# Optimization experiments

Hardware: AMD Instinct MI355X
Metric: run time of the kernel (lower is better)

Reference implementation:

```python
import jax, jax.numpy as jnp
import numpy as np
from jax import lax

H = 1024
NH = 16
R = 32
B, S = 32, 1024
LN_EPS = 1e-5

def _gelu(x):
    return jax.nn.gelu(x, approximate=False)

def setup_inputs() -> dict:
    key = jax.random.key(0)
    ks = jax.random.split(key, 24)
    w = lambda k, shape: jax.random.normal(k, shape, jnp.float32) * 0.02
    d = {}
    d['computation_results'] = jax.random.normal(ks[0], (B, S, H), jnp.float32)
    d['max_steps'] = 16
    # rule selector: Linear(H,H), GELU, Linear(H,R)
    d['rule_w1'] = w(ks[1], (H, H)); d['rule_b1'] = jnp.zeros((H,))
    d['rule_w2'] = w(ks[2], (R, H)); d['rule_b2'] = jnp.zeros((R,))
    d['rule_emb'] = jax.random.normal(ks[3], (R, H), jnp.float32)
    # MultiheadAttention packed in-proj [3H,H] and out-proj [H,H]
    d['attn_in_w'] = w(ks[4], (3 * H, H)); d['attn_in_b'] = jnp.zeros((3 * H,))
    d['attn_out_w'] = w(ks[5], (H, H)); d['attn_out_b'] = jnp.zeros((H,))
    # 2-layer LSTM, PyTorch gate order i,f,g,o
    d['lstm_wih0'] = w(ks[6], (4 * H, H)); d['lstm_whh0'] = w(ks[7], (4 * H, H))
    d['lstm_bih0'] = jnp.zeros((4 * H,)); d['lstm_bhh0'] = jnp.zeros((4 * H,))
    d['lstm_wih1'] = w(ks[8], (4 * H, H)); d['lstm_whh1'] = w(ks[9], (4 * H, H))
    d['lstm_bih1'] = jnp.zeros((4 * H,)); d['lstm_bhh1'] = jnp.zeros((4 * H,))
    # step generator: Linear(H,2H), LayerNorm(2H), GELU, Linear(2H,H)
    d['gen_w1'] = w(ks[10], (2 * H, H)); d['gen_b1'] = jnp.zeros((2 * H,))
    d['gen_ln_g'] = jnp.ones((2 * H,)); d['gen_ln_b'] = jnp.zeros((2 * H,))
    d['gen_w2'] = w(ks[11], (H, 2 * H)); d['gen_b2'] = jnp.zeros((H,))
    # step validator: Linear(2H,H), GELU, Linear(H,1), Sigmoid
    d['val_w1'] = w(ks[12], (H, 2 * H)); d['val_b1'] = jnp.zeros((H,))
    d['val_w2'] = w(ks[13], (1, H)); d['val_b2'] = jnp.zeros((1,))
    # proof verifier: Linear(H,H), GELU, Linear(H,1), Sigmoid
    d['ver_w1'] = w(ks[14], (H, H)); d['ver_b1'] = jnp.zeros((H,))
    d['ver_w2'] = w(ks[15], (1, H)); d['ver_b2'] = jnp.zeros((1,))
    return d


def reference(computation_results, max_steps, rule_w1, rule_b1, rule_w2, rule_b2, rule_emb,
              attn_in_w, attn_in_b, attn_out_w, attn_out_b,
              lstm_wih0, lstm_whh0, lstm_bih0, lstm_bhh0,
              lstm_wih1, lstm_whh1, lstm_bih1, lstm_bhh1,
              gen_w1, gen_b1, gen_ln_g, gen_ln_b, gen_w2, gen_b2,
              val_w1, val_b1, val_w2, val_b2,
              ver_w1, ver_b1, ver_w2, ver_b2):
    comp = computation_results
    b, s, h = comp.shape
    dh = h // NH
    scale = dh ** -0.5
    wq, wk, wv = jnp.split(attn_in_w, 3, axis=0)
    bq, bk, bv = jnp.split(attn_in_b, 3, axis=0)
    # K/V projections of the static context, computed once outside the step loop
    K = (comp @ wk.T + bk).reshape(b, s, NH, dh)  # [B,S,NH,dh]
    V = (comp @ wv.T + bv).reshape(b, s, NH, dh)
    lstm_params = ((lstm_wih0, lstm_whh0, lstm_bih0, lstm_bhh0),
                   (lstm_wih1, lstm_whh1, lstm_bih1, lstm_bhh1))

    def step(carry, _):
        ps, hmem, cmem = carry  # ps: [B,H]; hmem/cmem: [2,B,H]
        # rule selection
        logits = _gelu(ps @ rule_w1.T + rule_b1) @ rule_w2.T + rule_b2
        probs = jax.nn.softmax(logits, axis=-1)  # [B,R]
        sel = probs @ rule_emb  # [B,H]
        # single-query multi-head attention over computation context
        q = (ps @ wq.T + bq).reshape(b, NH, dh) * scale
        scores = jnp.einsum('bhd,bshd->bhs', q, K)
        a = jax.nn.softmax(scores, axis=-1)  # [B,NH,S]
        ctx = jnp.einsum('bhs,bshd->bhd', a, V).reshape(b, h) @ attn_out_w.T + attn_out_b
        attn_avg = a.mean(axis=1)  # head-averaged weights, [B,S]
        # 2-layer LSTM cell, one timestep
        x = ps
        hs, cs = [], []
        for l, (wih, whh, bih, bhh) in enumerate(lstm_params):
            g = x @ wih.T + bih + hmem[l] @ whh.T + bhh
            gi, gf, gg, go = jnp.split(g, 4, axis=-1)
            cn = jax.nn.sigmoid(gf) * cmem[l] + jax.nn.sigmoid(gi) * jnp.tanh(gg)
            hn = jax.nn.sigmoid(go) * jnp.tanh(cn)
            hs.append(hn); cs.append(cn); x = hn
        mem_out = x
        # step generator with LayerNorm+GELU
        si = ps + sel + ctx + mem_out
        z = si @ gen_w1.T + gen_b1
        mu = z.mean(axis=-1, keepdims=True)
        var = ((z - mu) ** 2).mean(axis=-1, keepdims=True)
        z = (z - mu) / jnp.sqrt(var + LN_EPS) * gen_ln_g + gen_ln_b
        nxt = _gelu(z) @ gen_w2.T + gen_b2
        val = jax.nn.sigmoid(_gelu(jnp.concatenate([ps, nxt], axis=-1) @ val_w1.T + val_b1) @ val_w2.T + val_b2)
        return (nxt, jnp.stack(hs), jnp.stack(cs)), (nxt, probs, val, attn_avg)

    init_state = comp[:, 0, :]
    carry0 = (init_state, jnp.zeros((2, b, h), comp.dtype), jnp.zeros((2, b, h), comp.dtype))
    (final, _, _), (steps, probs, vals, attn) = lax.scan(step, carry0, None, length=int(max_steps))
    proof_steps = jnp.concatenate([init_state[None], steps], axis=0)  # [T+1,B,H]
    proof_validity = jax.nn.sigmoid(_gelu(final @ ver_w1.T + ver_b1) @ ver_w2.T + ver_b2)  # [B,1]
    return proof_steps, proof_validity, probs, vals, attn
```

## Files before the change

kernel.cpp:

```cpp
#include <hip/hip_runtime.h>

typedef unsigned short u16;
typedef unsigned int u32;
typedef __attribute__((ext_vector_type(8))) short short8v;
typedef __attribute__((ext_vector_type(4))) float f32x4;

#define MFMA16(a,b,c) __builtin_amdgcn_mfma_f32_16x16x32_bf16((a),(b),(c),0,0,0)

__device__ __forceinline__ u16 f2bf(float f){
  u32 u = __float_as_uint(f);
  return (u16)((u + 0x7fffu + ((u >> 16) & 1u)) >> 16);
}
__device__ __forceinline__ float bf2f(u16 h){ return __uint_as_float(((u32)h) << 16); }
__device__ __forceinline__ float gelu_f(float x){ return 0.5f * x * (1.f + erff(x * 0.70710678118654752f)); }
__device__ __forceinline__ float sigm_f(float x){ return 1.f / (1.f + __expf(-x)); }
__device__ __forceinline__ void acc4(float4& a, const float4 b){ a.x+=b.x; a.y+=b.y; a.z+=b.z; a.w+=b.w; }

__device__ __forceinline__ void gl16(const void* g, void* l){
  __builtin_amdgcn_global_load_lds((const __attribute__((address_space(1))) u32*)g,
                                   (__attribute__((address_space(3))) u32*)l, 16, 0, 0);
}

struct CastJobs { const float* s[12]; u16* d[12]; int start[13]; };
__global__ __launch_bounds__(256) void cast_all_k(CastJobs J){
  int bx = blockIdx.x, j = 0;
  #pragma unroll
  for (int t = 0; t < 12; t++) if (bx >= J.start[t + 1]) j = t + 1;
  int i = (bx - J.start[j]) * 1024 + threadIdx.x * 4;
  float4 v = *(const float4*)(J.s[j] + i);
  ushort4 o; o.x = f2bf(v.x); o.y = f2bf(v.y); o.z = f2bf(v.z); o.w = f2bf(v.w);
  *(ushort4*)(J.d[j] + i) = o;
}

__global__ __launch_bounds__(256) void cast_k(const float* __restrict__ s, u16* __restrict__ d, int n){
  int i = (blockIdx.x * 256 + threadIdx.x) * 4;
  if (i + 3 < n){
    float4 v = *(const float4*)(s + i);
    ushort4 o; o.x = f2bf(v.x); o.y = f2bf(v.y); o.z = f2bf(v.z); o.w = f2bf(v.w);
    *(ushort4*)(d + i) = o;
  }
}

__global__ __launch_bounds__(256) void tcast_k(const float* __restrict__ s, u16* __restrict__ d){
  __shared__ float tile[32][33];
  int bx = blockIdx.x & 31, by = blockIdx.x >> 5;
  int tx = threadIdx.x & 31, ty = threadIdx.x >> 5;
  #pragma unroll
  for (int i = 0; i < 4; i++)
    tile[ty + i * 8][tx] = s[(size_t)(by * 32 + ty + i * 8) * 1024 + bx * 32 + tx];
  __syncthreads();
  #pragma unroll
  for (int i = 0; i < 4; i++)
    d[(size_t)(bx * 32 + ty + i * 8) * 1024 + by * 32 + tx] = f2bf(tile[tx][ty + i * 8]);
}

__global__ __launch_bounds__(256) void bias2_k(const float* __restrict__ gw1, const float* __restrict__ aob,
                                               const float* __restrict__ gb1, float* __restrict__ out){
  int j = blockIdx.x * 32 + (threadIdx.x >> 3);
  int l8 = threadIdx.x & 7;
  const float* r = gw1 + (size_t)j * 1024;
  float acc = 0.f;
  #pragma unroll 8
  for (int kk = 0; kk < 32; kk++){
    int k = kk * 32 + l8 * 4;
    float4 a = *(const float4*)(r + k);
    float4 w = *(const float4*)(aob + k);
    acc += a.x * w.x + a.y * w.y + a.z * w.z + a.w * w.w;
  }
  acc += __shfl_xor(acc, 1); acc += __shfl_xor(acc, 2); acc += __shfl_xor(acc, 4);
  if (l8 == 0) out[j] = gb1[j] + acc;
}

__global__ __launch_bounds__(256) void init_k(const float* __restrict__ comp, float* ps0, float* outp,
                                              float* h0, float* c0, float* h1, float* c1){
  int i = blockIdx.x * 256 + threadIdx.x;
  int b = i >> 10, hh = i & 1023;
  float v = comp[(size_t)b * 1048576 + hh];
  ps0[i] = v; outp[i] = v;
  h0[i] = 0.f; c0[i] = 0.f; h1[i] = 0.f; c1[i] = 0.f;
}

__global__ __launch_bounds__(256) void gemmkv_k(const u16* __restrict__ compb,
    const u16* __restrict__ Wk, const u16* __restrict__ Wv,
    const float* __restrict__ bk, const float* __restrict__ bv,
    u16* __restrict__ Kt, u16* __restrict__ Vb)
{
  __shared__ u16 Sh[16384];
  u16* As = Sh;
  u16* Bs = Sh + 8192;
  int tid = threadIdx.x;
  int x = blockIdx.x;
  int xcd = x & 7, p = x >> 3;
  int cpanel = xcd * 32 + (p >> 3);
  int wpanel = p & 7;
  int isK = (blockIdx.z != 0);
  const u16 *msrc, *nsrc; int m0, n0;
  if (!isK){ m0 = cpanel * 128; n0 = wpanel * 128; msrc = compb; nsrc = Wv; }
  else     { m0 = wpanel * 128; n0 = cpanel * 128; msrc = Wk;    nsrc = compb; }

  int w = tid >> 6, l = tid & 63, lr = l & 15, lk = l >> 4;
  int wm = (w >> 1) * 64, wn = (w & 1) * 64;
  f32x4 acc[4][4];
  #pragma unroll
  for (int i = 0; i < 4; i++)
    #pragma unroll
    for (int j = 0; j < 4; j++) acc[i][j] = (f32x4){0.f,0.f,0.f,0.f};

  for (int kc = 0; kc < 1024; kc += 64){
    #pragma unroll
    for (int r = 0; r < 4; r++){
      int s = tid + r * 256;
      int row = s >> 3, pp = s & 7;
      int lg = pp ^ (row & 7);
      gl16(msrc + (size_t)(m0 + row) * 1024 + kc + lg * 8, As + s * 8);
      gl16(nsrc + (size_t)(n0 + row) * 1024 + kc + lg * 8, Bs + s * 8);
    }
    __syncthreads();
    #pragma unroll
    for (int kk = 0; kk < 2; kk++){
      short8v a[4], bb[4];
      #pragma unroll
      for (int mi = 0; mi < 4; mi++){
        int row = wm + mi * 16 + lr;
        int ph = (kk * 4 + lk) ^ (row & 7);
        a[mi] = *(const short8v*)(As + row * 64 + ph * 8);
      }
      #pragma unroll
      for (int ni = 0; ni < 4; ni++){
        int row = wn + ni * 16 + lr;
        int ph = (kk * 4 + lk) ^ (row & 7);
        bb[ni] = *(const short8v*)(Bs + row * 64 + ph * 8);
      }
      #pragma unroll
      for (int mi = 0; mi < 4; mi++)
        #pragma unroll
        for (int ni = 0; ni < 4; ni++)
          acc[mi][ni] = MFMA16(a[mi], bb[ni], acc[mi][ni]);
    }
    __syncthreads();
  }
  #pragma unroll
  for (int mi = 0; mi < 4; mi++)
    #pragma unroll
    for (int ni = 0; ni < 4; ni++)
      #pragma unroll
      for (int r = 0; r < 4; r++){
        int row = wm + mi * 16 + lk * 4 + r;
        int col = wn + ni * 16 + lr;
        float bias = isK ? bk[m0 + row] : bv[n0 + col];
        Sh[row * 128 + col] = f2bf(acc[mi][ni][r] + bias);
      }
  __syncthreads();
  u16* dst = isK ? Kt : Vb;
  size_t base = isK ? (((size_t)(n0 >> 10) * 1024 + m0) * 1024 + (n0 & 1023))
                    : ((size_t)m0 * 1024 + n0);
  for (int i = tid; i < 2048; i += 256){
    int r = i >> 4, c8 = (i & 15) * 8;
    *(uint4*)(dst + base + (size_t)r * 1024 + c8) = *(const uint4*)(Sh + r * 128 + c8);
  }
}

__global__ __launch_bounds__(256) void gemmbb_k(const u16* __restrict__ A, const u16* __restrict__ B,
                                                u16* __restrict__ C)
{
  __shared__ u16 As[128 * 64];
  __shared__ u16 Bs[128 * 64];
  int tid = threadIdx.x;
  int m0 = blockIdx.x * 128, n0 = blockIdx.y * 128;
  int w = tid >> 6, l = tid & 63, lr = l & 15, lk = l >> 4;
  int wm = (w >> 1) * 64, wn = (w & 1) * 64;
  f32x4 acc[4][4];
  #pragma unroll
  for (int i = 0; i < 4; i++)
    #pragma unroll
    for (int j = 0; j < 4; j++) acc[i][j] = (f32x4){0.f,0.f,0.f,0.f};
  for (int kc = 0; kc < 1024; kc += 64){
    #pragma unroll
    for (int r = 0; r < 4; r++){
      int s = tid + r * 256;
      int row = s >> 3, pp = s & 7;
      int lg = pp ^ (row & 7);
      gl16(A + (size_t)(m0 + row) * 1024 + kc + lg * 8, As + s * 8);
      gl16(B + (size_t)(n0 + row) * 1024 + kc + lg * 8, Bs + s * 8);
    }
    __syncthreads();
    #pragma unroll
    for (int kk = 0; kk < 2; kk++){
      short8v a[4], bb[4];
      #pragma unroll
      for (int mi = 0; mi < 4; mi++){
        int row = wm + mi * 16 + lr;
        int ph = (kk * 4 + lk) ^ (row & 7);
        a[mi] = *(const short8v*)(As + row * 64 + ph * 8);
      }
      #pragma unroll
      for (int ni = 0; ni < 4; ni++){
        int row = wn + ni * 16 + lr;
        int ph = (kk * 4 + lk) ^ (row & 7);
        bb[ni] = *(const short8v*)(Bs + row * 64 + ph * 8);
      }
      #pragma unroll
      for (int mi = 0; mi < 4; mi++)
        #pragma unroll
        for (int ni = 0; ni < 4; ni++)
          acc[mi][ni] = MFMA16(a[mi], bb[ni], acc[mi][ni]);
    }
    __syncthreads();
  }
  #pragma unroll
  for (int mi = 0; mi < 4; mi++)
    #pragma unroll
    for (int ni = 0; ni < 4; ni++)
      #pragma unroll
      for (int r = 0; r < 4; r++){
        int row = m0 + wm + mi * 16 + lk * 4 + r;
        int col = n0 + wn + ni * 16 + lr;
        C[(size_t)row * 1024 + col] = f2bf(acc[mi][ni][r]);
      }
}

struct LinSeg {
  const float* X0; const float* Xa; const float* Xb; const float* Xc;
  const u16* W1; const float* b1;
  const float* Y; const u16* W2; const float* b2;
  float* out; float* out2;
  int K1, ld1, K2, ld2, N, act, gate;
  float scale;
  float* stats;
  const float* lng; const float* lnb; const float* lnstats;
  const float* cprev; float* cout; float* hout;
};

__device__ __forceinline__ short8v pack8(float4 v0, float4 v1){
  short8v r;
  r[0]=(short)f2bf(v0.x); r[1]=(short)f2bf(v0.y); r[2]=(short)f2bf(v0.z); r[3]=(short)f2bf(v0.w);
  r[4]=(short)f2bf(v1.x); r[5]=(short)f2bf(v1.y); r[6]=(short)f2bf(v1.z); r[7]=(short)f2bf(v1.w);
  return r;
}

__device__ __forceinline__ short8v load_sum8(const LinSeg& S, int row, int kb){
  size_t o = (size_t)row * S.K1 + kb;
  float4 v0 = *(const float4*)(S.X0 + o);
  float4 v1 = *(const float4*)(S.X0 + o + 4);
  if (S.lng){
    float mu = S.lnstats[row] * (1.f / 2048.f);
    float ms = S.lnstats[32 + row] * (1.f / 2048.f);
    float rstd = rsqrtf(ms - mu * mu + 1e-5f);
    float4 g0 = *(const float4*)(S.lng + kb), g1 = *(const float4*)(S.lng + kb + 4);
    float4 b0 = *(const float4*)(S.lnb + kb), b1 = *(const float4*)(S.lnb + kb + 4);
    v0.x = gelu_f((v0.x - mu) * rstd * g0.x + b0.x);
    v0.y = gelu_f((v0.y - mu) * rstd * g0.y + b0.y);
    v0.z = gelu_f((v0.z - mu) * rstd * g0.z + b0.z);
    v0.w = gelu_f((v0.w - mu) * rstd * g0.w + b0.w);
    v1.x = gelu_f((v1.x - mu) * rstd * g1.x + b1.x);
    v1.y = gelu_f((v1.y - mu) * rstd * g1.y + b1.y);
    v1.z = gelu_f((v1.z - mu) * rstd * g1.z + b1.z);
    v1.w = gelu_f((v1.w - mu) * rstd * g1.w + b1.w);
  } else {
    if (S.Xa){ acc4(v0, *(const float4*)(S.Xa + o)); acc4(v1, *(const float4*)(S.Xa + o + 4)); }
    if (S.Xb){ acc4(v0, *(const float4*)(S.Xb + o)); acc4(v1, *(const float4*)(S.Xb + o + 4)); }
    if (S.Xc){ acc4(v0, *(const float4*)(S.Xc + o)); acc4(v1, *(const float4*)(S.Xc + o + 4)); }
  }
  return pack8(v0, v1);
}
__device__ __forceinline__ short8v load_y8(const float* p){
  return pack8(*(const float4*)(p), *(const float4*)(p + 4));
}

typedef float Red4[32][32];

__device__ void lin_body(const LinSeg& S, int bi, int tid, Red4* red){
  int c0 = bi * 32, j0 = bi * 8;
  int w = tid >> 6, l = tid & 63, lr = l & 15, lk = l >> 4;
  int wc0 = S.gate ? ((lr >> 3) << 10) + j0 + (lr & 7) : c0 + lr;
  int wc1 = S.gate ? (((lr + 16) >> 3) << 10) + j0 + ((lr + 16) & 7) : c0 + lr + 16;
  f32x4 acc[2][2];
  #pragma unroll
  for (int i = 0; i < 2; i++)
    #pragma unroll
    for (int j = 0; j < 2; j++) acc[i][j] = (f32x4){0.f,0.f,0.f,0.f};

  {
    int chunk = S.K1 >> 2;
    int kb0 = w * chunk + lk * 8;
    for (int kk = 0; kk < chunk; kk += 32){
      int kb = kb0 + kk;
      short8v a0 = load_sum8(S, lr, kb);
      short8v a1 = load_sum8(S, lr + 16, kb);
      short8v w0 = *(const short8v*)(S.W1 + (size_t)wc0 * S.ld1 + kb);
      short8v w1 = *(const short8v*)(S.W1 + (size_t)wc1 * S.ld1 + kb);
      acc[0][0] = MFMA16(a0, w0, acc[0][0]);
      acc[0][1] = MFMA16(a0, w1, acc[0][1]);
      acc[1][0] = MFMA16(a1, w0, acc[1][0]);
      acc[1][1] = MFMA16(a1, w1, acc[1][1]);
    }
  }
  if (S.Y){
    int chunk = S.K2 >> 2;
    int kb0 = w * chunk + lk * 8;
    for (int kk = 0; kk < chunk; kk += 32){
      int kb = kb0 + kk;
      short8v a0 = load_y8(S.Y + (size_t)lr * S.K2 + kb);
      short8v a1 = load_y8(S.Y + (size_t)(lr + 16) * S.K2 + kb);
      short8v w0 = *(const short8v*)(S.W2 + (size_t)wc0 * S.ld2 + kb);
      short8v w1 = *(const short8v*)(S.W2 + (size_t)wc1 * S.ld2 + kb);
      acc[0][0] = MFMA16(a0, w0, acc[0][0]);
      acc[0][1] = MFMA16(a0, w1, acc[0][1]);
      acc[1][0] = MFMA16(a1, w0, acc[1][0]);
      acc[1][1] = MFMA16(a1, w1, acc[1][1]);
    }
  }
  #pragma unroll
  for (int mi = 0; mi < 2; mi++)
    #pragma unroll
    for (int ni = 0; ni < 2; ni++)
      #pragma unroll
      for (int r = 0; r < 4; r++)
        red[w][mi * 16 + lk * 4 + r][ni * 16 + lr] = acc[mi][ni][r];
  __syncthreads();
  if (S.gate){
    int row = tid >> 3, j = tid & 7;
    float s[4];
    #pragma unroll
    for (int g = 0; g < 4; g++){
      float v = 0.f;
      #pragma unroll
      for (int ww = 0; ww < 4; ww++) v += red[ww][row][g * 8 + j];
      s[g] = v;
    }
    int gc = j0 + j;
    float gI = s[0] + S.b1[gc]        + S.b2[gc];
    float gF = s[1] + S.b1[1024 + gc] + S.b2[1024 + gc];
    float gG = s[2] + S.b1[2048 + gc] + S.b2[2048 + gc];
    float gO = s[3] + S.b1[3072 + gc] + S.b2[3072 + gc];
    int idx = row * 1024 + gc;
    float cN = sigm_f(gF) * S.cprev[idx] + sigm_f(gI) * tanhf(gG);
    S.cout[idx] = cN;
    S.hout[idx] = sigm_f(gO) * tanhf(cN);
    return;
  }
  float vout[4]; int iout[4];
  int cnt = 0;
  for (int i = tid; i < 1024; i += 256){
    int row = i >> 5, col = i & 31;
    float v = 0.f;
    #pragma unroll
    for (int ww = 0; ww < 4; ww++) v += red[ww][row][col];
    v += S.b1[c0 + col];
    if (S.b2) v += S.b2[c0 + col];
    if (S.act == 1) v = gelu_f(v);
    else if (S.act == 2) v *= S.scale;
    S.out[(size_t)row * S.N + c0 + col] = v;
    if (S.out2) S.out2[(size_t)row * S.N + c0 + col] = v;
    vout[cnt] = v; iout[cnt] = i; cnt++;
  }
  if (S.stats){
    __syncthreads();
    float* rf = (float*)red;
    #pragma unroll
    for (int q2 = 0; q2 < 4; q2++){
      rf[iout[q2]] = vout[q2];
      rf[1024 + iout[q2]] = vout[q2] * vout[q2];
    }
    __syncthreads();
    if (tid < 32){
      float s = 0.f, s2 = 0.f;
      #pragma unroll
      for (int cc = 0; cc < 32; cc++){ s += rf[tid * 32 + cc]; s2 += rf[1024 + tid * 32 + cc]; }
      atomicAdd(S.stats + tid, s);
      atomicAdd(S.stats + 32 + tid, s2);
    }
  }
}

__global__ __launch_bounds__(256) void linmulti_k(LinSeg s0, LinSeg s1, LinSeg s2, int n0, int n1){
  __shared__ float red[4][32][32];
  int bx = blockIdx.x, tid = threadIdx.x;
  if (bx < n0) lin_body(s0, bx, tid, red);
  else if (bx < n0 + n1) lin_body(s1, bx - n0, tid, red);
  else lin_body(s2, bx - n0 - n1, tid, red);
}

__device__ void attn_job(int bh, int tid, const float* q, const u16* Kt, const u16* Vb,
                         float* afull, float* ctx0, float* shf){
  float* qs = shf;
  float* sc = shf + 64;
  float* rmx = shf + 1088;
  float* rsm = shf + 1092;
  float* ctxp = shf + 1096;
  int b = bh >> 4, h = bh & 15;
  if (tid < 64) qs[tid] = q[bh * 64 + tid];
  __syncthreads();
  const u32* kt = (const u32*)(Kt + (size_t)bh * 65536);
  float a0 = 0.f, a1 = 0.f, a2 = 0.f, a3 = 0.f;
  #pragma unroll 8
  for (int d = 0; d < 64; d++){
    float qd = qs[d];
    u32 p0 = kt[d * 512 + tid];
    u32 p1 = kt[d * 512 + tid + 256];
    a0 += qd * bf2f((u16)(p0 & 0xffff)); a1 += qd * bf2f((u16)(p0 >> 16));
    a2 += qd * bf2f((u16)(p1 & 0xffff)); a3 += qd * bf2f((u16)(p1 >> 16));
  }
  float mx = fmaxf(fmaxf(a0, a1), fmaxf(a2, a3));
  for (int o = 1; o < 64; o <<= 1) mx = fmaxf(mx, __shfl_xor(mx, o));
  if ((tid & 63) == 0) rmx[tid >> 6] = mx;
  __syncthreads();
  mx = fmaxf(fmaxf(rmx[0], rmx[1]), fmaxf(rmx[2], rmx[3]));
  float e0 = __expf(a0 - mx), e1 = __expf(a1 - mx), e2 = __expf(a2 - mx), e3 = __expf(a3 - mx);
  float sm = e0 + e1 + e2 + e3;
  for (int o = 1; o < 64; o <<= 1) sm += __shfl_xor(sm, o);
  if ((tid & 63) == 0) rsm[tid >> 6] = sm;
  __syncthreads();
  sm = rsm[0] + rsm[1] + rsm[2] + rsm[3];
  float inv = 1.f / sm;
  float* ar = afull + (size_t)bh * 1024;
  float2 w0 = make_float2(e0 * inv, e1 * inv);
  float2 w1 = make_float2(e2 * inv, e3 * inv);
  *(float2*)(sc + 2 * tid) = w0;       *(float2*)(ar + 2 * tid) = w0;
  *(float2*)(sc + 512 + 2 * tid) = w1; *(float2*)(ar + 512 + 2 * tid) = w1;
  __syncthreads();
  int d2 = (tid & 31) * 2, chunk = tid >> 5;
  const u16* vb = Vb + ((size_t)(b * 1024) * 16 + h) * 64 + d2;
  float c0 = 0.f, c1 = 0.f;
  for (int s = chunk * 128; s < chunk * 128 + 128; s++){
    u32 vv = *(const u32*)(vb + (size_t)s * 1024);
    float wv = sc[s];
    c0 += wv * bf2f((u16)(vv & 0xffff));
    c1 += wv * bf2f((u16)(vv >> 16));
  }
  *(float2*)(ctxp + chunk * 64 + d2) = make_float2(c0, c1);
  __syncthreads();
  if (tid < 64){
    float r = 0.f;
    #pragma unroll
    for (int c = 0; c < 8; c++) r += ctxp[c * 64 + tid];
    ctx0[bh * 64 + tid] = r;
  }
}

__device__ void rule2_job(int b, int tid, const float* h1a, const float* w2, const float* b2,
                          const float* emb, float* probs_out, float* sel, float* shf){
  float* lg = shf;
  float* psh = shf + 32;
  int j = tid >> 3, l8 = tid & 7;
  const float* xr = h1a + b * 1024;
  const float* wr = w2 + j * 1024;
  float acc = 0.f;
  #pragma unroll 8
  for (int kk = 0; kk < 32; kk++){
    int k = kk * 32 + l8 * 4;
    float4 xv = *(const float4*)(xr + k);
    float4 wv = *(const float4*)(wr + k);
    acc += xv.x * wv.x + xv.y * wv.y + xv.z * wv.z + xv.w * wv.w;
  }
  acc += __shfl_xor(acc, 1); acc += __shfl_xor(acc, 2); acc += __shfl_xor(acc, 4);
  if (l8 == 0) lg[j] = acc + b2[j];
  __syncthreads();
  if (tid < 32){
    float v = lg[tid];
    float m = v;
    for (int o = 1; o < 32; o <<= 1) m = fmaxf(m, __shfl_xor(m, o));
    float e = __expf(v - m);
    float s = e;
    for (int o = 1; o < 32; o <<= 1) s += __shfl_xor(s, o);
    float p = e / s;
    psh[tid] = p;
    probs_out[b * 32 + tid] = p;
  }
  __syncthreads();
  for (int j2 = tid; j2 < 1024; j2 += 256){
    float a2 = 0.f;
    #pragma unroll
    for (int r = 0; r < 32; r++) a2 += psh[r] * emb[r * 1024 + j2];
    sel[b * 1024 + j2] = a2;
  }
}

struct D2Params {
  const float* qbuf;
  const u16* Kt; const u16* Vb; float* afull; float* ctx0;
  const float* h1a; const float* w2; const float* b2r; const float* emb;
  float* probs_out; float* sel;
  LinSeg sL1; float* lnstats;
};
__global__ __launch_bounds__(256) void step_d2_k(D2Params P){
  __shared__ float red[4][32][32];
  float* shf = &red[0][0][0];
  int bx = blockIdx.x, tid = threadIdx.x;
  if (bx < 512){ attn_job(bx, tid, P.qbuf, P.Kt, P.Vb, P.afull, P.ctx0, shf); return; }
  if (bx < 544){ rule2_job(bx - 512, tid, P.h1a, P.w2, P.b2r, P.emb, P.probs_out, P.sel, shf); return; }
  if (bx < 672){ lin_body(P.sL1, bx - 544, tid, red); return; }
  if (tid < 64) P.lnstats[tid] = 0.f;
}

__global__ __launch_bounds__(256) void valver_k(const u16* __restrict__ vw1, const float* __restrict__ vb1,
    const u16* __restrict__ verw1, const float* __restrict__ verb1,
    const float* __restrict__ proof, float* __restrict__ v1){
  __shared__ float red[4][32][32];
  int t = blockIdx.y;
  LinSeg S = {};
  if (t < 16){
    S.X0 = proof + (size_t)t * 32768; S.K1 = 1024; S.W1 = vw1; S.ld1 = 2048; S.b1 = vb1;
    S.Y = proof + (size_t)(t + 1) * 32768; S.K2 = 1024; S.W2 = vw1 + 1024; S.ld2 = 2048;
  } else {
    S.X0 = proof + (size_t)16 * 32768; S.K1 = 1024; S.W1 = verw1; S.ld1 = 1024; S.b1 = verb1;
  }
  S.out = v1 + (size_t)t * 32768; S.N = 1024; S.act = 1;
  lin_body(S, blockIdx.x, threadIdx.x, red);
}

__global__ __launch_bounds__(256) void dotsig_b_k(const float* __restrict__ v1,
    const float* __restrict__ w2v, const float* __restrict__ b2v,
    const float* __restrict__ w2ver, const float* __restrict__ b2ver,
    float* __restrict__ out_vals, float* __restrict__ out_valid){
  int t = blockIdx.x;
  const float* w = (t < 16) ? w2v : w2ver;
  const float* bs = (t < 16) ? b2v : b2ver;
  const float* x = v1 + (size_t)t * 32768;
  int b = threadIdx.x >> 3, l8 = threadIdx.x & 7;
  const float* xr = x + (size_t)b * 1024;
  float acc = 0.f;
  #pragma unroll 8
  for (int kk = 0; kk < 32; kk++){
    int k = kk * 32 + l8 * 4;
    float4 xv = *(const float4*)(xr + k);
    float4 wv = *(const float4*)(w + k);
    acc += xv.x * wv.x + xv.y * wv.y + xv.z * wv.z + xv.w * wv.w;
  }
  acc += __shfl_xor(acc, 1); acc += __shfl_xor(acc, 2); acc += __shfl_xor(acc, 4);
  if (l8 == 0){
    float r = sigm_f(acc + bs[0]);
    if (t < 16) out_vals[t * 32 + b] = r; else out_valid[b] = r;
  }
}

__global__ __launch_bounds__(256) void attnavg_all_k(const float* __restrict__ afull, float* __restrict__ out){
  int idx = blockIdx.x * 256 + threadIdx.x;
  int t = idx >> 15, r = idx & 32767;
  int b = r >> 10, s = r & 1023;
  const float* base = afull + (size_t)t * 524288 + (size_t)b * 16384;
  float acc = 0.f;
  #pragma unroll
  for (int h = 0; h < 16; h++) acc += base[h * 1024 + s];
  out[idx] = acc * (1.f / 16.f);
}

extern "C" void kernel_launch(void* const* d_in, const int* in_sizes, int n_in,
                              void* d_out, int out_size, void* d_ws, size_t ws_size,
                              hipStream_t stream) {
  const float* comp      = (const float*)d_in[0];
  const float* rule_w1   = (const float*)d_in[2];
  const float* rule_b1   = (const float*)d_in[3];
  const float* rule_w2   = (const float*)d_in[4];
  const float* rule_b2   = (const float*)d_in[5];
  const float* rule_emb  = (const float*)d_in[6];
  const float* attn_in_w = (const float*)d_in[7];
  const float* attn_in_b = (const float*)d_in[8];
  const float* attn_out_w= (const float*)d_in[9];
  const float* attn_out_b= (const float*)d_in[10];
  const float* wih0 = (const float*)d_in[11];
  const float* whh0 = (const float*)d_in[12];
  const float* bih0 = (const float*)d_in[13];
  const float* bhh0 = (const float*)d_in[14];
  const float* wih1 = (const float*)d_in[15];
  const float* whh1 = (const float*)d_in[16];
  const float* bih1 = (const float*)d_in[17];
  const float* bhh1 = (const float*)d_in[18];
  const float* gen_w1 = (const float*)d_in[19];
  const float* gen_b1 = (const float*)d_in[20];
  const float* ln_g   = (const float*)d_in[21];
  const float* ln_b   = (const float*)d_in[22];
  const float* gen_w2 = (const float*)d_in[23];
  const float* gen_b2 = (const float*)d_in[24];
  const float* val_w1 = (const float*)d_in[25];
  const float* val_b1 = (const float*)d_in[26];
  const float* val_w2 = (const float*)d_in[27];
  const float* val_b2 = (const float*)d_in[28];
  const float* ver_w1 = (const float*)d_in[29];
  const float* ver_b1 = (const float*)d_in[30];
  const float* ver_w2 = (const float*)d_in[31];
  const float* ver_b2 = (const float*)d_in[32];

  float* out_f     = (float*)d_out;
  float* out_proof = out_f;
  float* out_valid = out_f + 17 * 32768;
  float* out_probs = out_valid + 32;
  float* out_vals  = out_probs + 16 * 1024;
  float* out_attn  = out_vals + 16 * 32;

  char* wp = (char*)d_ws;
  auto carve = [&](size_t bytes) -> void* {
    void* p = (void*)wp; wp += (bytes + 255) & ~(size_t)255; return p;
  };
  u16* Kt    = (u16*)carve((size_t)33554432 * 2);
  u16* Vb    = (u16*)carve((size_t)33554432 * 2);
  u16* compb = (u16*)carve((size_t)33554432 * 2);
  float* afull_all = (float*)compb;
  u16* rw1b  = (u16*)carve(2097152);
  u16* wqb   = (u16*)carve(2097152);
  u16* wkb   = (u16*)carve(2097152);
  u16* wvb   = (u16*)carve(2097152);
  u16* aowTb = (u16*)carve(2097152);
  u16* wih0b = (u16*)carve(8388608);
  u16* whh0b = (u16*)carve(8388608);
  u16* wih1b = (u16*)carve(8388608);
  u16* whh1b = (u16*)carve(8388608);
  u16* gw1b  = (u16*)carve(4194304);
  u16* gw2b  = (u16*)carve(4194304);
  u16* vw1b  = (u16*)carve(4194304);
  u16* verw1b= (u16*)carve(2097152);
  u16* gaw   = (u16*)carve(4194304);
  float* bias2 = (float*)carve(8192);
  float* psb[2]  = { (float*)carve(131072), (float*)carve(131072) };
  float* h0b[2]  = { (float*)carve(131072), (float*)carve(131072) };
  float* c0b[2]  = { (float*)carve(131072), (float*)carve(131072) };
  float* h1b[2]  = { (float*)carve(131072), (float*)carve(131072) };
  float* c1b[2]  = { (float*)carve(131072), (float*)carve(131072) };
  float* h1act = (float*)carve(131072);
  float* sel   = (float*)carve(131072);
  float* qbuf  = (float*)carve(131072);
  float* ctx0  = (float*)carve(131072);
  float* zbuf  = (float*)carve(262144);
  float* v1buf = (float*)carve(2228224);
  float* lnstats = (float*)carve(256);
  (void)ws_size; (void)in_sizes; (void)n_in; (void)out_size;

  CastJobs J;
  const float* srcs[12] = { rule_w1, attn_in_w, attn_in_w + 1048576, attn_in_w + 2097152,
                            wih0, whh0, wih1, whh1, gen_w1, gen_w2, val_w1, ver_w1 };
  u16* dsts[12] = { rw1b, wqb, wkb, wvb, wih0b, whh0b, wih1b, whh1b, gw1b, gw2b, vw1b, verw1b };
  int sizes[12] = { 1048576, 1048576, 1048576, 1048576,
                    4194304, 4194304, 4194304, 4194304, 2097152, 2097152, 2097152, 1048576 };
  int st = 0;
  for (int i = 0; i < 12; i++){ J.s[i] = srcs[i]; J.d[i] = dsts[i]; J.start[i] = st; st += sizes[i] / 1024; }
  J.start[12] = st;
  cast_all_k<<<dim3(st), dim3(256), 0, stream>>>(J);
  tcast_k<<<dim3(1024), dim3(256), 0, stream>>>(attn_out_w, aowTb);
  cast_k<<<dim3(32768), dim3(256), 0, stream>>>(comp, compb, 33554432);

  gemmkv_k<<<dim3(2048, 1, 2), dim3(256), 0, stream>>>(compb, wkb, wvb,
      attn_in_b + 1024, attn_in_b + 2048, Kt, Vb);
  gemmbb_k<<<dim3(16, 8), dim3(256), 0, stream>>>(gw1b, aowTb, gaw);
  bias2_k<<<dim3(64), dim3(256), 0, stream>>>(gen_w1, attn_out_b, gen_b1, bias2);

  init_k<<<dim3(128), dim3(256), 0, stream>>>(comp, psb[0], out_proof,
      h0b[0], c0b[0], h1b[0], c1b[0]);

  for (int t = 0; t < 16; t++){
    int cur = t & 1, nx = cur ^ 1;
    float* ps = psb[cur];
    float* afull_t = afull_all + (size_t)t * 524288;
    LinSeg sRule = {}; sRule.X0 = ps; sRule.K1 = 1024; sRule.W1 = rw1b; sRule.ld1 = 1024;
    sRule.b1 = rule_b1; sRule.out = h1act; sRule.N = 1024; sRule.act = 1;
    LinSeg sQ = {}; sQ.X0 = ps; sQ.K1 = 1024; sQ.W1 = wqb; sQ.ld1 = 1024; sQ.b1 = attn_in_b;
    sQ.out = qbuf; sQ.N = 1024; sQ.act = 2; sQ.scale = 0.125f;
    LinSeg sL0 = {}; sL0.X0 = ps; sL0.K1 = 1024; sL0.W1 = wih0b; sL0.ld1 = 1024; sL0.b1 = bih0;
    sL0.Y = h0b[cur]; sL0.K2 = 1024; sL0.W2 = whh0b; sL0.ld2 = 1024; sL0.b2 = bhh0;
    sL0.gate = 1; sL0.cprev = c0b[cur]; sL0.cout = c0b[nx]; sL0.hout = h0b[nx];
    linmulti_k<<<dim3(192), dim3(256), 0, stream>>>(sRule, sQ, sL0, 32, 32);
    D2Params P;
    P.qbuf = qbuf;
    P.Kt = Kt; P.Vb = Vb; P.afull = afull_t; P.ctx0 = ctx0;
    P.h1a = h1act; P.w2 = rule_w2; P.b2r = rule_b2; P.emb = rule_emb;
    P.probs_out = out_probs + t * 1024; P.sel = sel;
    LinSeg sL1 = {}; sL1.X0 = h0b[nx]; sL1.K1 = 1024; sL1.W1 = wih1b; sL1.ld1 = 1024; sL1.b1 = bih1;
    sL1.Y = h1b[cur]; sL1.K2 = 1024; sL1.W2 = whh1b; sL1.ld2 = 1024; sL1.b2 = bhh1;
    sL1.gate = 1; sL1.cprev = c1b[cur]; sL1.cout = c1b[nx]; sL1.hout = h1b[nx];
    P.sL1 = sL1; P.lnstats = lnstats;
    step_d2_k<<<dim3(673), dim3(256), 0, stream>>>(P);
    LinSeg sG1 = {}; sG1.X0 = ps; sG1.Xa = sel; sG1.Xb = h1b[nx];
    sG1.K1 = 1024; sG1.W1 = gw1b; sG1.ld1 = 1024; sG1.b1 = bias2;
    sG1.Y = ctx0; sG1.K2 = 1024; sG1.W2 = gaw; sG1.ld2 = 1024;
    sG1.out = zbuf; sG1.N = 2048; sG1.stats = lnstats;
    linmulti_k<<<dim3(64), dim3(256), 0, stream>>>(sG1, sG1, sG1, 64, 0);
    LinSeg sG2 = {}; sG2.X0 = zbuf; sG2.K1 = 2048; sG2.W1 = gw2b; sG2.ld1 = 2048; sG2.b1 = gen_b2;
    sG2.out = psb[nx]; sG2.N = 1024; sG2.out2 = out_proof + (size_t)(t + 1) * 32768;
    sG2.lng = ln_g; sG2.lnb = ln_b; sG2.lnstats = lnstats;
    linmulti_k<<<dim3(32), dim3(256), 0, stream>>>(sG2, sG2, sG2, 32, 0);
  }
  valver_k<<<dim3(32, 17), dim3(256), 0, stream>>>(vw1b, val_b1, verw1b, ver_b1, out_proof, v1buf);
  dotsig_b_k<<<dim3(17), dim3(256), 0, stream>>>(v1buf, val_w2, val_b2, ver_w2, ver_b2,
      out_vals, out_valid);
  attnavg_all_k<<<dim3(2048), dim3(256), 0, stream>>>(afull_all, out_attn);
}
```

Measured before the change: 2.105 ms.

## Store attention K and V cache as FP8 e4m3 with head-major V layout

The K/V projections are now encoded into a custom 8-bit e4m3-like format instead of bf16, halving the bytes the per-step attention kernel must stream from memory across all 16 steps. V is also rewritten into a head-contiguous [b,h,s,d] layout so each attention block reads contiguous rows, and the attention loops are reworked to decode four values per 32-bit load with 16 sequence chunks. This trades precision of K and V (3 mantissa bits, clamped range, flush of small values) for lower memory traffic, which may exceed the tolerance.

```diff
diff --git a/kernel.cpp b/kernel.cpp
--- a/kernel.cpp
+++ b/kernel.cpp
@@ -2,6 +2,7 @@
 
 typedef unsigned short u16;
 typedef unsigned int u32;
+typedef unsigned char u8;
 typedef __attribute__((ext_vector_type(8))) short short8v;
 typedef __attribute__((ext_vector_type(4))) float f32x4;
 
@@ -15,6 +16,21 @@
 __device__ __forceinline__ float gelu_f(float x){ return 0.5f * x * (1.f + erff(x * 0.70710678118654752f)); }
 __device__ __forceinline__ float sigm_f(float x){ return 1.f / (1.f + __expf(-x)); }
 __device__ __forceinline__ void acc4(float4& a, const float4 b){ a.x+=b.x; a.y+=b.y; a.z+=b.z; a.w+=b.w; }
+
+__device__ __forceinline__ u8 enc8(float f){
+  u32 u = __float_as_uint(f);
+  u32 s = (u >> 24) & 0x80u;
+  u32 mag = u & 0x7fffffffu;
+  if (mag > 0x43E00000u) mag = 0x43E00000u;
+  mag += 0x7ffffu + ((mag >> 20) & 1u);
+  int e = (int)(mag >> 23) - 120;
+  u32 m = (mag >> 20) & 7u;
+  if (e <= 0) return (u8)s;
+  return (u8)(s | ((u32)e << 3) | m);
+}
+__device__ __forceinline__ float dec8(u32 b){
+  return __uint_as_float(((b & 0x80u) << 24) | (((b & 0x7fu) << 20) + 0x3C000000u));
+}
 
 __device__ __forceinline__ void gl16(const void* g, void* l){
   __builtin_amdgcn_global_load_lds((const __attribute__((address_space(1))) u32*)g,
@@ -83,7 +99,7 @@
 __global__ __launch_bounds__(256) void gemmkv_k(const u16* __restrict__ compb,
     const u16* __restrict__ Wk, const u16* __restrict__ Wv,
     const float* __restrict__ bk, const float* __restrict__ bv,
-    u16* __restrict__ Kt, u16* __restrict__ Vb)
+    u8* __restrict__ K8, u8* __restrict__ V8)
 {
   __shared__ u16 Sh[16384];
   u16* As = Sh;
@@ -151,12 +167,30 @@
         Sh[row * 128 + col] = f2bf(acc[mi][ni][r] + bias);
       }
   __syncthreads();
-  u16* dst = isK ? Kt : Vb;
-  size_t base = isK ? (((size_t)(n0 >> 10) * 1024 + m0) * 1024 + (n0 & 1023))
-                    : ((size_t)m0 * 1024 + n0);
-  for (int i = tid; i < 2048; i += 256){
-    int r = i >> 4, c8 = (i & 15) * 8;
-    *(uint4*)(dst + base + (size_t)r * 1024 + c8) = *(const uint4*)(Sh + r * 128 + c8);
+  for (int i = tid; i < 1024; i += 256){
+    int r = i >> 3, c16 = (i & 7) * 16;
+    short8v s0 = *(const short8v*)(Sh + r * 128 + c16);
+    short8v s1 = *(const short8v*)(Sh + r * 128 + c16 + 8);
+    uint4 o;
+    u32 w0 = 0, w1 = 0, w2 = 0, w3 = 0;
+    #pragma unroll
+    for (int e = 0; e < 4; e++){
+      w0 |= (u32)enc8(bf2f((u16)s0[e]))     << (8 * e);
+      w1 |= (u32)enc8(bf2f((u16)s0[e + 4])) << (8 * e);
+      w2 |= (u32)enc8(bf2f((u16)s1[e]))     << (8 * e);
+      w3 |= (u32)enc8(bf2f((u16)s1[e + 4])) << (8 * e);
+    }
+    o.x = w0; o.y = w1; o.z = w2; o.w = w3;
+    if (!isK){
+      int bs = m0 + r, hd = n0 + c16;
+      int bb2 = bs >> 10, s = bs & 1023;
+      int hh = hd >> 6, dl = hd & 63;
+      *(uint4*)(V8 + (((size_t)(bb2 * 16 + hh) * 1024 + s) * 64 + dl)) = o;
+    } else {
+      int hd = m0 + r, bs = n0 + c16;
+      int bb2 = bs >> 10, s = bs & 1023;
+      *(uint4*)(K8 + ((size_t)(bb2 * 1024 + hd) * 1024 + s)) = o;
+    }
   }
 }
 
@@ -381,59 +415,61 @@
   else lin_body(s2, bx - n0 - n1, tid, red);
 }
 
-__device__ void attn_job(int bh, int tid, const float* q, const u16* Kt, const u16* Vb,
+__device__ void attn_job(int bh, int tid, const float* q, const u8* K8, const u8* V8,
                          float* afull, float* ctx0, float* shf){
   float* qs = shf;
   float* sc = shf + 64;
-  float* rmx = shf + 1088;
-  float* rsm = shf + 1092;
+  float* rr = shf + 1088;
   float* ctxp = shf + 1096;
   int b = bh >> 4, h = bh & 15;
   if (tid < 64) qs[tid] = q[bh * 64 + tid];
   __syncthreads();
-  const u32* kt = (const u32*)(Kt + (size_t)bh * 65536);
+  const u32* kt = (const u32*)(K8 + ((size_t)(b * 1024 + h * 64)) * 1024);
   float a0 = 0.f, a1 = 0.f, a2 = 0.f, a3 = 0.f;
   #pragma unroll 8
   for (int d = 0; d < 64; d++){
     float qd = qs[d];
-    u32 p0 = kt[d * 512 + tid];
-    u32 p1 = kt[d * 512 + tid + 256];
-    a0 += qd * bf2f((u16)(p0 & 0xffff)); a1 += qd * bf2f((u16)(p0 >> 16));
-    a2 += qd * bf2f((u16)(p1 & 0xffff)); a3 += qd * bf2f((u16)(p1 >> 16));
+    u32 p = kt[d * 256 + tid];
+    a0 += qd * dec8(p & 0xffu);
+    a1 += qd * dec8((p >> 8) & 0xffu);
+    a2 += qd * dec8((p >> 16) & 0xffu);
+    a3 += qd * dec8(p >> 24);
   }
   float mx = fmaxf(fmaxf(a0, a1), fmaxf(a2, a3));
   for (int o = 1; o < 64; o <<= 1) mx = fmaxf(mx, __shfl_xor(mx, o));
-  if ((tid & 63) == 0) rmx[tid >> 6] = mx;
-  __syncthreads();
-  mx = fmaxf(fmaxf(rmx[0], rmx[1]), fmaxf(rmx[2], rmx[3]));
+  if ((tid & 63) == 0) rr[tid >> 6] = mx;
+  __syncthreads();
+  mx = fmaxf(fmaxf(rr[0], rr[1]), fmaxf(rr[2], rr[3]));
   float e0 = __expf(a0 - mx), e1 = __expf(a1 - mx), e2 = __expf(a2 - mx), e3 = __expf(a3 - mx);
   float sm = e0 + e1 + e2 + e3;
   for (int o = 1; o < 64; o <<= 1) sm += __shfl_xor(sm, o);
-  if ((tid & 63) == 0) rsm[tid >> 6] = sm;
-  __syncthreads();
-  sm = rsm[0] + rsm[1] + rsm[2] + rsm[3];
+  if ((tid & 63) == 0) rr[4 + (tid >> 6)] = sm;
+  __syncthreads();
+  sm = rr[4] + rr[5] + rr[6] + rr[7];
   float inv = 1.f / sm;
-  float* ar = afull + (size_t)bh * 1024;
-  float2 w0 = make_float2(e0 * inv, e1 * inv);
-  float2 w1 = make_float2(e2 * inv, e3 * inv);
-  *(float2*)(sc + 2 * tid) = w0;       *(float2*)(ar + 2 * tid) = w0;
-  *(float2*)(sc + 512 + 2 * tid) = w1; *(float2*)(ar + 512 + 2 * tid) = w1;
-  __syncthreads();
-  int d2 = (tid & 31) * 2, chunk = tid >> 5;
-  const u16* vb = Vb + ((size_t)(b * 1024) * 16 + h) * 64 + d2;
-  float c0 = 0.f, c1 = 0.f;
-  for (int s = chunk * 128; s < chunk * 128 + 128; s++){
-    u32 vv = *(const u32*)(vb + (size_t)s * 1024);
-    float wv = sc[s];
-    c0 += wv * bf2f((u16)(vv & 0xffff));
-    c1 += wv * bf2f((u16)(vv >> 16));
-  }
-  *(float2*)(ctxp + chunk * 64 + d2) = make_float2(c0, c1);
+  float4 wv = make_float4(e0 * inv, e1 * inv, e2 * inv, e3 * inv);
+  *(float4*)(sc + 4 * tid) = wv;
+  *(float4*)(afull + (size_t)bh * 1024 + 4 * tid) = wv;
+  __syncthreads();
+  int dd = (tid & 15) * 4, chunk = tid >> 4;
+  const u32* vp = (const u32*)(V8 + (((size_t)(b * 16 + h) * 1024 + chunk * 64) * 64 + dd));
+  const float* scp = sc + chunk * 64;
+  float c0 = 0.f, c1 = 0.f, c2 = 0.f, c3 = 0.f;
+  #pragma unroll 8
+  for (int s = 0; s < 64; s++){
+    u32 vv = vp[s * 16];
+    float w = scp[s];
+    c0 += w * dec8(vv & 0xffu);
+    c1 += w * dec8((vv >> 8) & 0xffu);
+    c2 += w * dec8((vv >> 16) & 0xffu);
+    c3 += w * dec8(vv >> 24);
+  }
+  *(float4*)(ctxp + chunk * 64 + dd) = make_float4(c0, c1, c2, c3);
   __syncthreads();
   if (tid < 64){
     float r = 0.f;
     #pragma unroll
-    for (int c = 0; c < 8; c++) r += ctxp[c * 64 + tid];
+    for (int c = 0; c < 16; c++) r += ctxp[c * 64 + tid];
     ctx0[bh * 64 + tid] = r;
   }
 }
@@ -478,7 +514,7 @@
 
 struct D2Params {
   const float* qbuf;
-  const u16* Kt; const u16* Vb; float* afull; float* ctx0;
+  const u8* K8; const u8* V8; float* afull; float* ctx0;
   const float* h1a; const float* w2; const float* b2r; const float* emb;
   float* probs_out; float* sel;
   LinSeg sL1; float* lnstats;
@@ -487,7 +523,7 @@
   __shared__ float red[4][32][32];
   float* shf = &red[0][0][0];
   int bx = blockIdx.x, tid = threadIdx.x;
-  if (bx < 512){ attn_job(bx, tid, P.qbuf, P.Kt, P.Vb, P.afull, P.ctx0, shf); return; }
+  if (bx < 512){ attn_job(bx, tid, P.qbuf, P.K8, P.V8, P.afull, P.ctx0, shf); return; }
   if (bx < 544){ rule2_job(bx - 512, tid, P.h1a, P.w2, P.b2r, P.emb, P.probs_out, P.sel, shf); return; }
   if (bx < 672){ lin_body(P.sL1, bx - 544, tid, red); return; }
   if (tid < 64) P.lnstats[tid] = 0.f;
@@ -592,8 +628,8 @@
   auto carve = [&](size_t bytes) -> void* {
     void* p = (void*)wp; wp += (bytes + 255) & ~(size_t)255; return p;
   };
-  u16* Kt    = (u16*)carve((size_t)33554432 * 2);
-  u16* Vb    = (u16*)carve((size_t)33554432 * 2);
+  u8* K8     = (u8*)carve((size_t)33554432);
+  u8* V8     = (u8*)carve((size_t)33554432);
   u16* compb = (u16*)carve((size_t)33554432 * 2);
   float* afull_all = (float*)compb;
   u16* rw1b  = (u16*)carve(2097152);
@@ -639,7 +675,7 @@
   cast_k<<<dim3(32768), dim3(256), 0, stream>>>(comp, compb, 33554432);
 
   gemmkv_k<<<dim3(2048, 1, 2), dim3(256), 0, stream>>>(compb, wkb, wvb,
-      attn_in_b + 1024, attn_in_b + 2048, Kt, Vb);
+      attn_in_b + 1024, attn_in_b + 2048, K8, V8);
   gemmbb_k<<<dim3(16, 8), dim3(256), 0, stream>>>(gw1b, aowTb, gaw);
   bias2_k<<<dim3(64), dim3(256), 0, stream>>>(gen_w1, attn_out_b, gen_b1, bias2);
 
@@ -660,7 +696,7 @@
     linmulti_k<<<dim3(192), dim3(256), 0, stream>>>(sRule, sQ, sL0, 32, 32);
     D2Params P;
     P.qbuf = qbuf;
-    P.Kt = Kt; P.Vb = Vb; P.afull = afull_t; P.ctx0 = ctx0;
+    P.K8 = K8; P.V8 = V8; P.afull = afull_t; P.ctx0 = ctx0;
     P.h1a = h1act; P.w2 = rule_w2; P.b2r = rule_b2; P.emb = rule_emb;
     P.probs_out = out_probs + t * 1024; P.sel = sel;
     LinSeg sL1 = {}; sL1.X0 = h0b[nx]; sL1.K1 = 1024; sL1.W1 = wih1b; sL1.ld1 = 1024; sL1.b1 = bih1;
```

New measurement: 2.117 ms. No clear change (+0.6%).
